# Optimization experiments

Measured on AMD Instinct MI355X. Metric: run time of the kernel, lower is better.

Reference implementation:

```python
import jax, jax.numpy as jnp
import numpy as np


def setup_inputs() -> dict:
    key = jax.random.key(0)
    ks = jax.random.split(key, 7)
    B, I, H = 8192, 1024, 1024
    x = jax.random.normal(ks[0], (B, I), dtype=jnp.float32)
    h_prev = jax.random.normal(ks[1], (B, H), dtype=jnp.float32)
    C_prev = jax.random.normal(ks[2], (B, H), dtype=jnp.float32)
    W_f = jax.random.normal(ks[3], (I + H, H), dtype=jnp.float32) * 0.01
    W_i = jax.random.normal(ks[4], (I + H, H), dtype=jnp.float32) * 0.01
    W_C = jax.random.normal(ks[5], (I + H, H), dtype=jnp.float32) * 0.01
    W_o = jax.random.normal(ks[6], (I + H, H), dtype=jnp.float32) * 0.01
    b = jnp.zeros((H,), dtype=jnp.float32)
    return {"x": x, "h_prev": h_prev, "C_prev": C_prev,
            "W_f": W_f, "b_f": b, "W_i": W_i, "b_i": b,
            "W_C": W_C, "b_C": b, "W_o": W_o, "b_o": b}


def reference(x, h_prev, C_prev, W_f, b_f, W_i, b_i, W_C, b_C, W_o, b_o):
    combined = jnp.concatenate([x, h_prev], axis=1)  # [B, I+H]
    # Fuse the four gate GEMMs into one [B, I+H] x [I+H, 4H] matmul.
    W = jnp.concatenate([W_f, W_i, W_o, W_C], axis=1)  # [I+H, 4H]
    b = jnp.concatenate([b_f, b_i, b_o, b_C], axis=0)  # [4H]
    gates = combined @ W + b                            # [B, 4H]
    H = C_prev.shape[1]
    f_t = jax.nn.sigmoid(gates[:, 0:H])
    i_t = jax.nn.sigmoid(gates[:, H:2 * H])
    o_t = jax.nn.sigmoid(gates[:, 2 * H:3 * H])
    C_tilda = jnp.tanh(gates[:, 3 * H:4 * H])
    C_t = f_t * C_prev + i_t * C_tilda
    h_t = o_t * jnp.tanh(C_t)
    return (h_t, C_t)
```

## Files before the change

### kernel.cpp

```cpp
#include <hip/hip_runtime.h>
#include <hip/hip_bf16.h>

#define B_SZ 8192
#define IH   2048
#define H_SZ 1024
#define BM   256
#define BK   64
#define NT   (IH / BK)
#define NI   (NT / 2)
#define DBUF 65536
#define WOFF 32768

typedef __attribute__((ext_vector_type(8))) short  short8;
typedef __attribute__((ext_vector_type(4))) float  floatx4;

static __device__ __forceinline__ ushort f2bf(float f) {
  union { float f; unsigned u; } v; v.f = f;
  unsigned u = v.u;
  u += 0x7fffu + ((u >> 16) & 1u);
  return (ushort)(u >> 16);
}
static __device__ __forceinline__ float sigmoidf_(float x) {
  return 1.0f / (1.0f + __expf(-x));
}
static __device__ __forceinline__ float tanhf_(float x) {
  float ax = fabsf(x);
  float e = __expf(-2.0f * ax);
  float t = (1.0f - e) / (1.0f + e);
  return copysignf(t, x);
}
static __device__ __forceinline__ void gload_lds16(const void* gsrc, void* ldst) {
  __builtin_amdgcn_global_load_lds(
      (__attribute__((address_space(1))) const void*)gsrc,
      (__attribute__((address_space(3))) void*)ldst, 16, 0, 0);
}

__global__ __launch_bounds__(256) void convert_w_kernel(
    const float* __restrict__ Wf, const float* __restrict__ Wi,
    const float* __restrict__ Wo, const float* __restrict__ Wc,
    ushort* __restrict__ Wt) {
  __shared__ float tile[64][65];
  const int g  = blockIdx.z;
  const float* W = (g == 0) ? Wf : (g == 1) ? Wi : (g == 2) ? Wo : Wc;
  const int n0 = blockIdx.x * 64;
  const int k0 = blockIdx.y * 64;
  const int tid = threadIdx.x;
#pragma unroll
  for (int i = 0; i < 4; ++i) {
    int c = i * 256 + tid;
    int r = c >> 4, c4 = c & 15;
    float4 v = *(const float4*)(W + (size_t)(k0 + r) * H_SZ + n0 + c4 * 4);
    tile[r][c4 * 4 + 0] = v.x;
    tile[r][c4 * 4 + 1] = v.y;
    tile[r][c4 * 4 + 2] = v.z;
    tile[r][c4 * 4 + 3] = v.w;
  }
  __syncthreads();
  const int n  = tid >> 2;
  const int kc = (tid & 3) * 16;
  ushort o[16] __attribute__((aligned(16)));
#pragma unroll
  for (int e = 0; e < 16; ++e) o[e] = f2bf(tile[kc + e][n]);
  ushort* dst = Wt + ((size_t)g * H_SZ + n0 + n) * IH + k0 + kc;
  *(uint4*)(dst)     = *(uint4*)&o[0];
  *(uint4*)(dst + 8) = *(uint4*)&o[8];
}

__global__ __launch_bounds__(256) void convert_a_kernel(
    const float* __restrict__ x, const float* __restrict__ hp,
    ushort* __restrict__ Abf) {
  size_t idx = ((size_t)blockIdx.x * 256 + threadIdx.x) * 8;
  size_t row = idx >> 11;
  size_t col = idx & 2047;
  const float* src = (col < 1024) ? (x  + row * 1024 + col)
                                  : (hp + row * 1024 + (col - 1024));
  float4 v0 = *(const float4*)(src);
  float4 v1 = *(const float4*)(src + 4);
  ushort o[8] __attribute__((aligned(16)));
  o[0] = f2bf(v0.x); o[1] = f2bf(v0.y); o[2] = f2bf(v0.z); o[3] = f2bf(v0.w);
  o[4] = f2bf(v1.x); o[5] = f2bf(v1.y); o[6] = f2bf(v1.z); o[7] = f2bf(v1.w);
  *(uint4*)(Abf + idx) = *(uint4*)&o[0];
}

__global__ __launch_bounds__(512, 2) void lstm_fused_kernel(
    const float* __restrict__ Cp, const ushort* __restrict__ Wt,
    const ushort* __restrict__ Abf,
    const float* __restrict__ bf_, const float* __restrict__ bi_,
    const float* __restrict__ bo_, const float* __restrict__ bc_,
    float* __restrict__ out) {
  __shared__ char lds[2 * DBUF];

  const int bid = blockIdx.x;
  const int wg  = (bid & 7) * 64 + (bid >> 3);
  const int b0  = (wg >> 4) * BM;
  const int n0g = (wg & 15) * 64;

  const int tid = threadIdx.x;
  const int ln  = tid & 63;
  const int wv  = tid >> 6;
  const int wm  = wv >> 1, wn = wv & 1;

  floatx4 acc[4][8];
#pragma unroll
  for (int m = 0; m < 4; ++m)
#pragma unroll
    for (int j = 0; j < 8; ++j) acc[m][j] = {0.f, 0.f, 0.f, 0.f};

  const int sw = (ln & 7) << 4;
  int kb[2];
  kb[0] = (((ln >> 4) << 4)) ^ sw;
  kb[1] = (64 + ((ln >> 4) << 4)) ^ sw;
  int arow[4], brow[8];
#pragma unroll
  for (int mf = 0; mf < 4; ++mf)
    arow[mf] = (wm * 64 + mf * 16 + (ln & 15)) * 128;
#pragma unroll
  for (int j = 0; j < 8; ++j) {
    int g = j >> 1, ns = j & 1;
    brow[j] = WOFF + (g * 64 + wn * 32 + ns * 16 + (ln & 15)) * 128;
  }

  const int    kcsw = ((tid & 7) * 16) ^ (((tid >> 3) & 7) << 4);
  const char*  AbfB = (const char*)Abf;
  const char*  WtB  = (const char*)Wt;
  size_t aoff[2];
#pragma unroll
  for (int i = 0; i < 2; ++i)
    aoff[i] = ((size_t)(b0 + i * 64 + (tid >> 3)) << 12) + kcsw;
  size_t woff[2][2];
#pragma unroll
  for (int h = 0; h < 2; ++h)
#pragma unroll
    for (int i = 0; i < 2; ++i) {
      int nrt  = h * 128 + i * 64 + (tid >> 3);
      int g    = nrt >> 6, nloc = nrt & 63;
      woff[h][i] = ((size_t)(g * H_SZ + n0g + nloc) << 12) + kcsw;
    }
  int dsto[2];
#pragma unroll
  for (int i = 0; i < 2; ++i) dsto[i] = (i * 512 + wv * 64) * 16;

#define STAGE_A(db, ktb, h)                                                   \
  do {                                                                        \
    gload_lds16(AbfB + aoff[0] + ((size_t)(h) << 19) + (ktb),                 \
                lds + (db) + (h) * 16384 + dsto[0]);                          \
    gload_lds16(AbfB + aoff[1] + ((size_t)(h) << 19) + (ktb),                 \
                lds + (db) + (h) * 16384 + dsto[1]);                          \
  } while (0)
#define STAGE_W(db, ktb, h)                                                   \
  do {                                                                        \
    gload_lds16(WtB + woff[h][0] + (ktb),                                     \
                lds + (db) + WOFF + (h) * 16384 + dsto[0]);                   \
    gload_lds16(WtB + woff[h][1] + (ktb),                                     \
                lds + (db) + WOFF + (h) * 16384 + dsto[1]);                   \
  } while (0)

  short8 aF[4][2];
  short8 bF[8][2];
#define RD_A(db, mf)                                                          \
  do {                                                                        \
    aF[mf][0] = *(const short8*)(lds + (db) + arow[mf] + kb[0]);              \
    aF[mf][1] = *(const short8*)(lds + (db) + arow[mf] + kb[1]);              \
  } while (0)
#define RD_B(db, j)                                                           \
  do {                                                                        \
    bF[j][0] = *(const short8*)(lds + (db) + brow[j] + kb[0]);                \
    bF[j][1] = *(const short8*)(lds + (db) + brow[j] + kb[1]);                \
  } while (0)
#define MFQ(mh, jh)                                                           \
  do {                                                                        \
    __builtin_amdgcn_s_setprio(1);                                            \
    _Pragma("unroll")                                                         \
    for (int mf_ = 2 * (mh); mf_ < 2 * (mh) + 2; ++mf_)                       \
      _Pragma("unroll")                                                       \
      for (int j_ = 4 * (jh); j_ < 4 * (jh) + 4; ++j_) {                      \
        acc[mf_][j_] = __builtin_amdgcn_mfma_f32_16x16x32_bf16(               \
            aF[mf_][0], bF[j_][0], acc[mf_][j_], 0, 0, 0);                    \
        acc[mf_][j_] = __builtin_amdgcn_mfma_f32_16x16x32_bf16(               \
            aF[mf_][1], bF[j_][1], acc[mf_][j_], 0, 0, 0);                    \
      }                                                                       \
    __builtin_amdgcn_s_setprio(0);                                            \
  } while (0)
#define BAR   __builtin_amdgcn_s_barrier()
#define LGKM0                                                                 \
  do {                                                                        \
    asm volatile("s_waitcnt lgkmcnt(0)" ::: "memory");                        \
    __builtin_amdgcn_sched_barrier(0);                                        \
  } while (0)
#define VMC6  asm volatile("s_waitcnt vmcnt(6)" ::: "memory")

  STAGE_W(0, 0, 0); STAGE_A(0, 0, 0); STAGE_A(0, 0, 1); STAGE_W(0, 0, 1);
  STAGE_W(DBUF, 128, 0); STAGE_A(DBUF, 128, 0); STAGE_A(DBUF, 128, 1);
  VMC6;
  BAR;

#pragma unroll 1
  for (int it = 0; it < NI; ++it) {
    const int kt1b  = (2 * it + 1) * 128;
    const int ktn0b = ((2 * it + 2) & 31) * 128;
    const int ktn1b = ((2 * it + 3) & 31) * 128;
    RD_A(0, 0); RD_A(0, 1);
    RD_B(0, 0); RD_B(0, 1); RD_B(0, 2); RD_B(0, 3);
    STAGE_W(DBUF, kt1b, 1);
    BAR; LGKM0; MFQ(0, 0); BAR;
    RD_A(0, 2); RD_A(0, 3);
    STAGE_W(0, ktn0b, 0);
    BAR; LGKM0; MFQ(1, 0); BAR;
    RD_B(0, 4); RD_B(0, 5); RD_B(0, 6); RD_B(0, 7);
    STAGE_A(0, ktn0b, 0);
    BAR; LGKM0; MFQ(0, 1); BAR;
    STAGE_A(0, ktn0b, 1);
    BAR; LGKM0; MFQ(1, 1);
    VMC6; BAR;
    RD_A(DBUF, 0); RD_A(DBUF, 1);
    RD_B(DBUF, 0); RD_B(DBUF, 1); RD_B(DBUF, 2); RD_B(DBUF, 3);
    STAGE_W(0, ktn0b, 1);
    BAR; LGKM0; MFQ(0, 0); BAR;
    RD_A(DBUF, 2); RD_A(DBUF, 3);
    STAGE_W(DBUF, ktn1b, 0);
    BAR; LGKM0; MFQ(1, 0); BAR;
    RD_B(DBUF, 4); RD_B(DBUF, 5); RD_B(DBUF, 6); RD_B(DBUF, 7);
    STAGE_A(DBUF, ktn1b, 0);
    BAR; LGKM0; MFQ(0, 1); BAR;
    STAGE_A(DBUF, ktn1b, 1);
    BAR; LGKM0; MFQ(1, 1);
    VMC6; BAR;
  }

  const int colq = ln & 15;
  const int rq   = ln >> 4;
  float* outh = out;
  float* outC = out + (size_t)B_SZ * H_SZ;
#pragma unroll
  for (int mf = 0; mf < 4; ++mf) {
#pragma unroll
    for (int ns = 0; ns < 2; ++ns) {
      int n = n0g + wn * 32 + ns * 16 + colq;
      float vbf = bf_[n], vbi = bi_[n], vbo = bo_[n], vbc = bc_[n];
#pragma unroll
      for (int r = 0; r < 4; ++r) {
        int row = b0 + wm * 64 + mf * 16 + rq * 4 + r;
        float fg = sigmoidf_(acc[mf][0 + ns][r] + vbf);
        float ig = sigmoidf_(acc[mf][2 + ns][r] + vbi);
        float og = sigmoidf_(acc[mf][4 + ns][r] + vbo);
        float cg = tanhf_  (acc[mf][6 + ns][r] + vbc);
        float cp = Cp[(size_t)row * H_SZ + n];
        float Ct = fg * cp + ig * cg;
        float ht = og * tanhf_(Ct);
        outh[(size_t)row * H_SZ + n] = ht;
        outC[(size_t)row * H_SZ + n] = Ct;
      }
    }
  }
#undef STAGE_A
#undef STAGE_W
#undef RD_A
#undef RD_B
#undef MFQ
#undef BAR
#undef LGKM0
#undef VMC6
}

extern "C" void kernel_launch(void* const* d_in, const int* in_sizes, int n_in,
                              void* d_out, int out_size, void* d_ws, size_t ws_size,
                              hipStream_t stream) {
  const float* x  = (const float*)d_in[0];
  const float* hp = (const float*)d_in[1];
  const float* Cp = (const float*)d_in[2];
  const float* Wf = (const float*)d_in[3];
  const float* bf = (const float*)d_in[4];
  const float* Wi = (const float*)d_in[5];
  const float* bi = (const float*)d_in[6];
  const float* Wc = (const float*)d_in[7];
  const float* bc = (const float*)d_in[8];
  const float* Wo = (const float*)d_in[9];
  const float* bo = (const float*)d_in[10];

  ushort* Wt  = (ushort*)d_ws;
  ushort* Abf = (ushort*)((char*)d_ws + (16u << 20));

  dim3 gridT(16, 32, 4);
  convert_w_kernel<<<gridT, 256, 0, stream>>>(Wf, Wi, Wo, Wc, Wt);
  convert_a_kernel<<<8192, 256, 0, stream>>>(x, hp, Abf);

  lstm_fused_kernel<<<512, 512, 0, stream>>>(Cp, Wt, Abf,
                                             bf, bi, bo, bc, (float*)d_out);
}
```

Measured before the change: 168.8 us.

## Software-pipeline LDS fragment reads one quadrant ahead of the MFMA blocks

Restructures the main loop so that the LDS reads for the next MFMA quadrant are issued before the current quadrant's MFMAs run. Full lgkmcnt(0) waits become partial waits, so fragment loads overlap with matrix math. The first quadrant's reads for each k-tile are hoisted into the previous phase and into a prologue. The vmcnt waits also move so the next buffer's reads can start earlier. The cost is more careful register-liveness ordering and a redundant read on the final iteration.

Result: slower. 356.2 us (+111.0%).

```diff
diff --git a/kernel.cpp b/kernel.cpp
--- a/kernel.cpp
+++ b/kernel.cpp
@@ -167,6 +167,11 @@
     bF[j][0] = *(const short8*)(lds + (db) + brow[j] + kb[0]);                \
     bF[j][1] = *(const short8*)(lds + (db) + brow[j] + kb[1]);                \
   } while (0)
+#define RDQ0(db)                                                              \
+  do { RD_A(db, 0); RD_A(db, 1);                                              \
+       RD_B(db, 0); RD_B(db, 1); RD_B(db, 2); RD_B(db, 3); } while (0)
+#define RDQ1(db)  do { RD_A(db, 2); RD_A(db, 3); } while (0)
+#define RDQ2(db)  do { RD_B(db, 4); RD_B(db, 5); RD_B(db, 6); RD_B(db, 7); } while (0)
 #define MFQ(mh, jh)                                                           \
   do {                                                                        \
     __builtin_amdgcn_s_setprio(1);                                            \
@@ -182,49 +187,40 @@
     __builtin_amdgcn_s_setprio(0);                                            \
   } while (0)
 #define BAR   __builtin_amdgcn_s_barrier()
-#define LGKM0                                                                 \
-  do {                                                                        \
-    asm volatile("s_waitcnt lgkmcnt(0)" ::: "memory");                        \
+#define LGKM(n)                                                               \
+  do {                                                                        \
+    asm volatile("s_waitcnt lgkmcnt(" #n ")" ::: "memory");                   \
     __builtin_amdgcn_sched_barrier(0);                                        \
   } while (0)
-#define VMC6  asm volatile("s_waitcnt vmcnt(6)" ::: "memory")
+#define VMC(n) asm volatile("s_waitcnt vmcnt(" #n ")" ::: "memory")
 
   STAGE_W(0, 0, 0); STAGE_A(0, 0, 0); STAGE_A(0, 0, 1); STAGE_W(0, 0, 1);
   STAGE_W(DBUF, 128, 0); STAGE_A(DBUF, 128, 0); STAGE_A(DBUF, 128, 1);
-  VMC6;
+  VMC(6);
   BAR;
+  RDQ0(0);
 
 #pragma unroll 1
   for (int it = 0; it < NI; ++it) {
     const int kt1b  = (2 * it + 1) * 128;
     const int ktn0b = ((2 * it + 2) & 31) * 128;
     const int ktn1b = ((2 * it + 3) & 31) * 128;
-    RD_A(0, 0); RD_A(0, 1);
-    RD_B(0, 0); RD_B(0, 1); RD_B(0, 2); RD_B(0, 3);
-    STAGE_W(DBUF, kt1b, 1);
-    BAR; LGKM0; MFQ(0, 0); BAR;
-    RD_A(0, 2); RD_A(0, 3);
-    STAGE_W(0, ktn0b, 0);
-    BAR; LGKM0; MFQ(1, 0); BAR;
-    RD_B(0, 4); RD_B(0, 5); RD_B(0, 6); RD_B(0, 7);
+    RDQ1(0); STAGE_W(DBUF, kt1b, 1);
+    BAR; LGKM(4);  MFQ(0, 0); BAR;
+    RDQ2(0); STAGE_W(0, ktn0b, 0);
+    BAR; LGKM(8);  MFQ(1, 0); BAR;
     STAGE_A(0, ktn0b, 0);
-    BAR; LGKM0; MFQ(0, 1); BAR;
-    STAGE_A(0, ktn0b, 1);
-    BAR; LGKM0; MFQ(1, 1);
-    VMC6; BAR;
-    RD_A(DBUF, 0); RD_A(DBUF, 1);
-    RD_B(DBUF, 0); RD_B(DBUF, 1); RD_B(DBUF, 2); RD_B(DBUF, 3);
-    STAGE_W(0, ktn0b, 1);
-    BAR; LGKM0; MFQ(0, 0); BAR;
-    RD_A(DBUF, 2); RD_A(DBUF, 3);
-    STAGE_W(DBUF, ktn1b, 0);
-    BAR; LGKM0; MFQ(1, 0); BAR;
-    RD_B(DBUF, 4); RD_B(DBUF, 5); RD_B(DBUF, 6); RD_B(DBUF, 7);
+    BAR; LGKM(0);  MFQ(0, 1); VMC(4); BAR;
+    RDQ0(DBUF); STAGE_A(0, ktn0b, 1);
+    BAR; LGKM(12); MFQ(1, 1); BAR;
+    RDQ1(DBUF); STAGE_W(0, ktn0b, 1);
+    BAR; LGKM(4);  MFQ(0, 0); BAR;
+    RDQ2(DBUF); STAGE_W(DBUF, ktn1b, 0);
+    BAR; LGKM(8);  MFQ(1, 0); BAR;
     STAGE_A(DBUF, ktn1b, 0);
-    BAR; LGKM0; MFQ(0, 1); BAR;
-    STAGE_A(DBUF, ktn1b, 1);
-    BAR; LGKM0; MFQ(1, 1);
-    VMC6; BAR;
+    BAR; LGKM(0);  MFQ(0, 1); VMC(4); BAR;
+    RDQ0(0); STAGE_A(DBUF, ktn1b, 1);
+    BAR; LGKM(12); MFQ(1, 1); BAR;
   }
 
   const int colq = ln & 15;
@@ -256,10 +252,13 @@
 #undef STAGE_W
 #undef RD_A
 #undef RD_B
+#undef RDQ0
+#undef RDQ1
+#undef RDQ2
 #undef MFQ
 #undef BAR
-#undef LGKM0
-#undef VMC6
+#undef LGKM
+#undef VMC
 }
 
 extern "C" void kernel_launch(void* const* d_in, const int* in_sizes, int n_in,
```
